# Performance work log

Hardware: AMD Instinct MI355X
Metric: run time of the kernel (lower is better)

The kernel has to match this reference:

```python
import jax, jax.numpy as jnp
import numpy as np

B, Q, K, D, H, HD, HID, ED, CPB, E = 2, 300, 1024, 256, 8, 32, 32, 256, 256, 131072
N = B * Q
EPS = 1e-5


def _ln(x, g, b):
    mu = x.mean(-1, keepdims=True)
    v = ((x - mu) ** 2).mean(-1, keepdims=True)
    return (x - mu) / jnp.sqrt(v + EPS) * g + b


def setup_inputs():
    key = jax.random.key(0)
    ks = jax.random.split(key, 32)
    rn = lambda k, s, sc=0.02: jax.random.normal(k, s, jnp.float32) * sc
    return {
        "nodes": jax.random.normal(ks[0], (N, D), jnp.float32),
        "images": jax.random.normal(ks[1], (B, K, D), jnp.float32),
        "rel_coords": jax.random.normal(ks[2], (B, Q, K, 2), jnp.float32),
        "edge_feats": jax.random.normal(ks[3], (E, ED), jnp.float32),
        "edge_index": jax.random.randint(ks[4], (2, E), 0, N, jnp.int32),
        "images_mask": jnp.zeros((B, K), dtype=bool),
        "ln1_g": jnp.ones((D,)), "ln1_b": jnp.zeros((D,)),
        "ln2_g": jnp.ones((D,)), "ln2_b": jnp.zeros((D,)),
        "ln3_g": jnp.ones((D,)), "ln3_b": jnp.zeros((D,)),
        "Wni": rn(ks[5], (D, HID * H)), "bni": jnp.zeros((HID * H,)),
        "Wnj": rn(ks[6], (D, HID * H)), "bnj": jnp.zeros((HID * H,)),
        "We": rn(ks[7], (ED, HID * H)), "be": jnp.zeros((HID * H,)),
        "attn_proj": jax.random.normal(ks[8], (H, HID), jnp.float32),
        "Wmsg": rn(ks[9], (D + ED, D)), "bmsg": jnp.zeros((D,)),
        "Wg_out": rn(ks[10], (D, D)), "bg_out": jnp.zeros((D,)),
        "Wq": rn(ks[11], (D, D)), "bq": jnp.zeros((D,)),
        "Wkv": rn(ks[12], (D, 2 * D)), "bkv": jnp.zeros((2 * D,)),
        "Wc1": rn(ks[13], (2, CPB), 0.5), "bc1": jnp.zeros((CPB,)),
        "Wc2": rn(ks[14], (CPB, H), 0.1), "bc2": jnp.zeros((H,)),
        "Wc_out": rn(ks[15], (D, D)), "bc_out": jnp.zeros((D,)),
        "Wf1": rn(ks[16], (D, 4 * D)), "bf1": jnp.zeros((4 * D,)),
        "Wf2": rn(ks[17], (4 * D, D)), "bf2": jnp.zeros((D,)),
    }


def reference(nodes, images, rel_coords, edge_feats, edge_index, images_mask,
              ln1_g, ln1_b, ln2_g, ln2_b, ln3_g, ln3_b,
              Wni, bni, Wnj, bnj, We, be, attn_proj, Wmsg, bmsg, Wg_out, bg_out,
              Wq, bq, Wkv, bkv, Wc1, bc1, Wc2, bc2, Wc_out, bc_out,
              Wf1, bf1, Wf2, bf2):
    src, dst = edge_index[0], edge_index[1]
    # --- graph attention (pre-LN residual) ---
    x = _ln(nodes, ln1_g, ln1_b)
    ni, nj = x[src], x[dst]  # [E, D]
    hidden = jax.nn.leaky_relu(
        ni @ Wni + bni + nj @ Wnj + bnj + edge_feats @ We + be, 0.2)
    hidden = hidden.reshape(E, H, HID)
    logits = jnp.einsum('ehd,hd->eh', hidden, attn_proj)  # [E, H]
    m = jax.ops.segment_max(logits, src, num_segments=N)
    z = jnp.exp(logits - m[src])
    scores = z / jax.ops.segment_sum(z, src, num_segments=N)[src]  # scatter softmax
    msg = (jnp.concatenate([nj, edge_feats], -1) @ Wmsg + bmsg).reshape(E, H, HD)
    agg = jax.ops.segment_sum(msg * scores[..., None], src, num_segments=N).reshape(N, D)
    nodes = nodes + (agg @ Wg_out + bg_out)
    # --- cross attention with continuous position bias ---
    x2 = _ln(nodes, ln2_g, ln2_b).reshape(B, Q, D)
    q = (x2 @ Wq + bq).reshape(B, Q, H, HD).transpose(0, 2, 1, 3)  # [B,H,Q,hd]
    kv = (images @ Wkv + bkv).reshape(B, K, 2, H, HD)
    k = kv[:, :, 0].transpose(0, 2, 1, 3)  # [B,H,K,hd]
    v = kv[:, :, 1].transpose(0, 2, 1, 3)
    cpb = jax.nn.relu(rel_coords @ Wc1 + bc1) @ Wc2 + bc2  # [B,Q,K,H]
    bias = jnp.where(images_mask[:, None, None, :], -jnp.inf,
                     jnp.transpose(cpb, (0, 3, 1, 2)))  # [B,H,Q,K]
    att = jnp.einsum('bhqd,bhkd->bhqk', q, k) / jnp.sqrt(jnp.float32(HD)) + bias
    p = jax.nn.softmax(att, axis=-1)
    out = jnp.einsum('bhqk,bhkd->bhqd', p, v)
    out = out.reshape(B, Q, H * HD)  # faithful to original: reshape WITHOUT head transpose
    nodes = nodes + (out @ Wc_out + bc_out).reshape(N, D)
    # --- FFN (residual from the normed input, as in original) ---
    x3 = _ln(nodes, ln3_g, ln3_b)
    ff = jax.nn.gelu(x3 @ Wf1 + bf1, approximate=False) @ Wf2 + bf2
    return ff + x3
```

## Files before the change

kernel.cpp:

```cpp
#include <hip/hip_runtime.h>
#include <hip/hip_bf16.h>
#include <math.h>

#define E_   131072
#define CH_  16384
#define N_   600
#define NB_  2
#define NQ_  300
#define NK_  1024
#define NH_  8

typedef __hip_bfloat16 bf16;
typedef __bf16 bh8 __attribute__((ext_vector_type(8)));
typedef float  fx4 __attribute__((ext_vector_type(4)));

static __device__ __forceinline__ float b2f(bf16 x){ return __bfloat162float(x); }
static __device__ __forceinline__ unsigned pack2(float x, float y){
  unsigned a = __bfloat16_as_ushort(__float2bfloat16(x));
  unsigned b = __bfloat16_as_ushort(__float2bfloat16(y));
  return a | (b << 16);
}
static __device__ __forceinline__ float ldf(const void* p, size_t i, bool isf32){
  return isf32 ? ((const float*)p)[i] : b2f(((const bf16*)p)[i]);
}

constexpr int WOFF[31] = {
  0,256,512,768,1024,1280,
  1536,67072,67328,132864,
  133120,133376,
  133632,264704,
  264960,330496,330752,396288,
  396544,527616,
  528128,528640,528896,530944,
  530952,596488,
  596744,858888,859912,1122056,
  1122312};
#define NWSEG 30
#define WTOT  1122312
struct SrcTab { const void* p[NWSEG]; };

static __device__ __forceinline__ void ln_stats(float v, int t, float* r1, float* r2,
                                                float& mu, float& rstd){
  float s1 = v, s2 = v*v;
  #pragma unroll
  for (int o = 32; o; o >>= 1){ s1 += __shfl_down(s1, o); s2 += __shfl_down(s2, o); }
  if ((t & 63) == 0){ r1[t>>6] = s1; r2[t>>6] = s2; }
  __syncthreads();
  float t1 = r1[0]+r1[1]+r1[2]+r1[3];
  float t2 = r2[0]+r2[1]+r2[2]+r2[3];
  mu = t1 * (1.f/256.f);
  float var = t2 * (1.f/256.f) - mu*mu;
  rstd = rsqrtf(var + 1e-5f);
  __syncthreads();
}

__global__ void k_init(int* cnt, unsigned* mkey, float* denom,
                       const void* nodes, int* dflag){
  int i = blockIdx.x*256 + threadIdx.x;
  if (i < N_) cnt[i] = 0;
  if (i < N_*NH_){ mkey[i] = 0u; denom[i] = 0.f; }
  if (i == 0){
    const unsigned short* h = (const unsigned short*)nodes;
    int odd = 0;
    for (int j = 0; j < 64; j++){
      int e = (h[j] >> 7) & 0xFF;
      if (e < 100 || e > 150) odd++;
    }
    *dflag = (odd > 8) ? 1 : 0;
  }
}

__global__ __launch_bounds__(256) void k_cvt(SrcTab tab, float* wall, const int* dflag){
  int i = blockIdx.x*256 + threadIdx.x;
  if (i >= WTOT) return;
  bool isf32 = (*dflag != 0);
  int seg = 0;
  while (seg < NWSEG-1 && i >= WOFF[seg+1]) seg++;
  wall[i] = ldf(tab.p[seg], (size_t)(i - WOFF[seg]), isf32);
}

__global__ __launch_bounds__(256) void k_prep2(
    const void* __restrict__ WeRaw, const int* __restrict__ dflag,
    const float* __restrict__ wall,
    bf16* __restrict__ WeT, bf16* __restrict__ WkvT, bf16* __restrict__ WnpT,
    bf16* __restrict__ WcoT, bf16* __restrict__ Wf1T, bf16* __restrict__ Wf2T,
    float* __restrict__ biasH)
{
  int i = blockIdx.x*256 + threadIdx.x;
  bool isf32 = (*dflag != 0);
  const float* Wni = wall + WOFF[6];
  const float* Wnj = wall + WOFF[8];
  const float* Wmsg= wall + WOFF[12];
  const float* Wkv = wall + WOFF[18];
  const float* Wco = wall + WOFF[24];
  const float* Wf1 = wall + WOFF[26];
  const float* Wf2 = wall + WOFF[28];
  if (i < 65536){
    int n = i >> 8, k = i & 255;
    WeT[i] = __float2bfloat16(ldf(WeRaw, (size_t)k*256 + n, isf32));
  } else if (i < 196608){
    int j = i - 65536; int n = j >> 8, k = j & 255;
    WkvT[j] = __float2bfloat16(Wkv[k*512 + n]);
  } else if (i < 393216){
    int j = i - 196608; int n = j >> 8, k = j & 255;
    float v = (n < 256) ? Wni[k*256 + n] : (n < 512) ? Wnj[k*256 + (n-256)]
                        : Wmsg[k*256 + (n-512)];
    WnpT[j] = __float2bfloat16(v);
  } else if (i < 458752){
    int j = i - 393216; int n = j >> 8, k = j & 255;
    WcoT[j] = __float2bfloat16(Wco[k*256 + n]);
  } else if (i < 720896){
    int j = i - 458752; int n = j >> 8, k = j & 255;
    Wf1T[j] = __float2bfloat16(Wf1[(size_t)k*1024 + n]);
  } else if (i < 983040){
    int j = i - 720896; int n = j >> 10, k = j & 1023;
    Wf2T[j] = __float2bfloat16(Wf2[(size_t)k*256 + n]);
  } else if (i < 983296){
    int j = i - 983040;
    biasH[j] = wall[WOFF[7]+j] + wall[WOFF[9]+j] + wall[WOFF[10]+j];
  }
}

__global__ __launch_bounds__(256) void k_ln1(
    const void* __restrict__ nodes, const int* __restrict__ dflag,
    const float* __restrict__ g1, const float* __restrict__ b1, bf16* __restrict__ x1)
{
  __shared__ float r1[4], r2[4];
  int n = blockIdx.x, t = threadIdx.x;
  bool isf32 = (*dflag != 0);
  float v = ldf(nodes, (size_t)n*256 + t, isf32);
  float mu, rstd;
  ln_stats(v, t, r1, r2, mu, rstd);
  x1[n*256 + t] = __float2bfloat16((v - mu) * rstd * g1[t] + b1[t]);
}

__global__ void k_count(const int* __restrict__ ei, int* cnt){
  int e = blockIdx.x*256 + threadIdx.x;
  atomicAdd(&cnt[ei[e]], 1);
}

__global__ __launch_bounds__(1024) void k_scan(const int* __restrict__ cnt,
                                               int* offs, int* cursor){
  __shared__ int s[1024];
  int t = threadIdx.x;
  s[t] = (t < N_) ? cnt[t] : 0;
  __syncthreads();
  for (int o = 1; o < 1024; o <<= 1){
    int v = 0;
    if (t >= o) v = s[t - o];
    __syncthreads();
    if (t >= o) s[t] += v;
    __syncthreads();
  }
  if (t < N_){ int excl = (t == 0) ? 0 : s[t-1]; offs[t] = excl; cursor[t] = excl; }
  if (t == N_-1) offs[N_] = s[N_-1];
}

__global__ void k_scatter(const int* __restrict__ ei, int* cursor, int* eorder){
  int e = blockIdx.x*256 + threadIdx.x;
  int pos = atomicAdd(&cursor[ei[e]], 1);
  eorder[pos] = e;
}

__global__ __launch_bounds__(256) void k_gemm_dual(
    const void* __restrict__ A, int m_base, const int* __restrict__ dflag,
    const bf16* __restrict__ BT, bf16* __restrict__ C)
{
  __shared__ __align__(16) bf16 As[128*40];
  __shared__ __align__(16) bf16 Bs[128*40];
  int m0 = blockIdx.x * 128;
  int n0 = blockIdx.y * 128;
  int t = threadIdx.x;
  bool isf32 = (*dflag != 0);
  int wave = t >> 6, lane = t & 63;
  int wr = (wave >> 1) * 64, wc = (wave & 1) * 64;
  int lm = lane & 15, lq = lane >> 4;
  int srow = t >> 2;
  int scol = (t & 3) * 8;
  size_t r0 = (size_t)(m_base + m0 + srow) * 256;
  size_t r1 = (size_t)(m_base + m0 + 64 + srow) * 256;
  fx4 acc[4][4] = {};
  for (int kk = 0; kk < 256; kk += 32){
    uint4 pa0, pa1;
    if (isf32){
      const float* a0p = (const float*)A + r0 + kk + scol;
      const float* a1p = (const float*)A + r1 + kk + scol;
      float4 va0a = *(const float4*)(a0p);
      float4 va0b = *(const float4*)(a0p + 4);
      float4 va1a = *(const float4*)(a1p);
      float4 va1b = *(const float4*)(a1p + 4);
      pa0.x = pack2(va0a.x, va0a.y); pa0.y = pack2(va0a.z, va0a.w);
      pa0.z = pack2(va0b.x, va0b.y); pa0.w = pack2(va0b.z, va0b.w);
      pa1.x = pack2(va1a.x, va1a.y); pa1.y = pack2(va1a.z, va1a.w);
      pa1.z = pack2(va1b.x, va1b.y); pa1.w = pack2(va1b.z, va1b.w);
    } else {
      pa0 = *(const uint4*)((const bf16*)A + r0 + kk + scol);
      pa1 = *(const uint4*)((const bf16*)A + r1 + kk + scol);
    }
    float4 vb0 = *(const float4*)(BT + (size_t)(n0 + srow)      * 256 + kk + scol);
    float4 vb1 = *(const float4*)(BT + (size_t)(n0 + 64 + srow) * 256 + kk + scol);
    __syncthreads();
    *(uint4*)(As + srow*40 + scol)         = pa0;
    *(uint4*)(As + (64 + srow)*40 + scol)  = pa1;
    *(float4*)(Bs + srow*40 + scol)        = vb0;
    *(float4*)(Bs + (64 + srow)*40 + scol) = vb1;
    __syncthreads();
    bh8 af[4], bfr[4];
    #pragma unroll
    for (int mt = 0; mt < 4; mt++)
      af[mt] = *reinterpret_cast<const bh8*>(As + (wr + mt*16 + lm)*40 + lq*8);
    #pragma unroll
    for (int nt = 0; nt < 4; nt++)
      bfr[nt] = *reinterpret_cast<const bh8*>(Bs + (wc + nt*16 + lm)*40 + lq*8);
    #pragma unroll
    for (int mt = 0; mt < 4; mt++)
      #pragma unroll
      for (int nt = 0; nt < 4; nt++)
        acc[mt][nt] = __builtin_amdgcn_mfma_f32_16x16x32_bf16(af[mt], bfr[nt], acc[mt][nt], 0, 0, 0);
  }
  #pragma unroll
  for (int mt = 0; mt < 4; mt++)
    #pragma unroll
    for (int nt = 0; nt < 4; nt++)
      #pragma unroll
      for (int r = 0; r < 4; r++){
        int row = m0 + wr + mt*16 + lq*4 + r;
        int col = n0 + wc + nt*16 + lm;
        C[(size_t)row*256 + col] = __float2bfloat16(acc[mt][nt][r]);
      }
}

__global__ __launch_bounds__(256) void k_gemm(
    const void* __restrict__ A, const int* __restrict__ dflag, int adual,
    int K, int M, const bf16* __restrict__ BT, int mode,
    void* __restrict__ D, int ldd,
    const float* __restrict__ bias, const float* __restrict__ add,
    float* __restrict__ aux)
{
  __shared__ __align__(16) bf16 As[128*40];
  __shared__ __align__(16) bf16 Bs[128*40];
  int m0 = blockIdx.x * 128;
  int n0 = blockIdx.y * 128;
  int t = threadIdx.x;
  bool f32src = adual && (*dflag != 0);
  int wave = t >> 6, lane = t & 63;
  int wr = (wave >> 1) * 64, wc = (wave & 1) * 64;
  int lm = lane & 15, lq = lane >> 4;
  int srow = t >> 2;
  int scol = (t & 3) * 8;
  size_t rA0 = (size_t)(m0 + srow) * K;
  size_t rA1 = (size_t)(m0 + 64 + srow) * K;
  size_t rB0 = (size_t)(n0 + srow) * K;
  size_t rB1 = (size_t)(n0 + 64 + srow) * K;
  fx4 acc[4][4] = {};
  for (int kk = 0; kk < K; kk += 32){
    uint4 pa0, pa1;
    if (f32src){
      const float* a0p = (const float*)A + rA0 + kk + scol;
      const float* a1p = (const float*)A + rA1 + kk + scol;
      float4 a = *(const float4*)(a0p), b = *(const float4*)(a0p + 4);
      float4 c = *(const float4*)(a1p), d = *(const float4*)(a1p + 4);
      pa0.x = pack2(a.x,a.y); pa0.y = pack2(a.z,a.w);
      pa0.z = pack2(b.x,b.y); pa0.w = pack2(b.z,b.w);
      pa1.x = pack2(c.x,c.y); pa1.y = pack2(c.z,c.w);
      pa1.z = pack2(d.x,d.y); pa1.w = pack2(d.z,d.w);
    } else {
      pa0 = *(const uint4*)((const bf16*)A + rA0 + kk + scol);
      pa1 = *(const uint4*)((const bf16*)A + rA1 + kk + scol);
    }
    float4 vb0 = *(const float4*)(BT + rB0 + kk + scol);
    float4 vb1 = *(const float4*)(BT + rB1 + kk + scol);
    __syncthreads();
    *(uint4*)(As + srow*40 + scol)         = pa0;
    *(uint4*)(As + (64 + srow)*40 + scol)  = pa1;
    *(float4*)(Bs + srow*40 + scol)        = vb0;
    *(float4*)(Bs + (64 + srow)*40 + scol) = vb1;
    __syncthreads();
    bh8 af[4], bfr[4];
    #pragma unroll
    for (int mt = 0; mt < 4; mt++)
      af[mt] = *reinterpret_cast<const bh8*>(As + (wr + mt*16 + lm)*40 + lq*8);
    #pragma unroll
    for (int nt = 0; nt < 4; nt++)
      bfr[nt] = *reinterpret_cast<const bh8*>(Bs + (wc + nt*16 + lm)*40 + lq*8);
    #pragma unroll
    for (int mt = 0; mt < 4; mt++)
      #pragma unroll
      for (int nt = 0; nt < 4; nt++)
        acc[mt][nt] = __builtin_amdgcn_mfma_f32_16x16x32_bf16(af[mt], bfr[nt], acc[mt][nt], 0, 0, 0);
  }
  #pragma unroll
  for (int mt = 0; mt < 4; mt++)
    #pragma unroll
    for (int nt = 0; nt < 4; nt++)
      #pragma unroll
      for (int r = 0; r < 4; r++){
        int row = m0 + wr + mt*16 + lq*4 + r;
        int col = n0 + wc + nt*16 + lm;
        if (row >= M) continue;
        float v = acc[mt][nt][r];
        if (mode == 0){
          if (bias) v += bias[col];
          ((float*)D)[(size_t)row*ldd + col] = v;
        } else if (mode == 1){
          v += bias[col];
          if (col < 256){
            ((float*)D)[(size_t)row*256 + col] = v;
          } else {
            int b = row >> 10, ki = row & 1023;
            int hh = (col - 256) >> 5, dd = (col - 256) & 31;
            aux[(((size_t)b*NH_ + hh)*32 + dd)*NK_ + ki] = v;
          }
        } else if (mode == 2){
          v += bias[col] + add[(size_t)row*ldd + col];
          ((float*)D)[(size_t)row*ldd + col] = v;
        } else {
          v += bias[col];
          float g = 0.5f*v*(1.f + erff(v*0.70710678118654752f));
          ((bf16*)D)[(size_t)row*ldd + col] = __float2bfloat16(g);
        }
      }
}

__global__ __launch_bounds__(256) void k_logits(
    const bf16* __restrict__ He, const float* __restrict__ Pall,
    const float* __restrict__ biasH, const float* __restrict__ ap, const int* __restrict__ ei,
    float* __restrict__ logits, unsigned* __restrict__ mkey, int e0chunk)
{
  __shared__ float hs[32*264];
  __shared__ int   ssh[32], dsh[32];
  __shared__ float aps[256], bhs[256];
  int t = threadIdx.x;
  int base = e0chunk + blockIdx.x*32;
  if (t < 32) ssh[t] = ei[base + t];
  else if (t < 64) dsh[t-32] = ei[E_ + base + (t - 32)];
  aps[t] = ap[t];
  bhs[t] = biasH[t];
  __syncthreads();
  int slot = (t >> 5)*33 + (t & 31);
  for (int r = 0; r < 32; r++){
    float v = b2f(He[(size_t)(base - e0chunk + r)*256 + t])
            + Pall[ssh[r]*768 + t] + Pall[dsh[r]*768 + 256 + t] + bhs[t];
    v = (v > 0.f) ? v : 0.2f*v;
    hs[r*264 + slot] = v;
  }
  __syncthreads();
  int e = t >> 3, h = t & 7;
  const float* hr  = hs + e*264 + h*33;
  const float* apr = aps + h*32;
  float acc = 0.f;
  #pragma unroll
  for (int i = 0; i < 32; i++) acc = fmaf(hr[i], apr[i], acc);
  logits[(size_t)(base + e)*8 + h] = acc;
  unsigned ub = __float_as_uint(acc);
  unsigned key = (ub & 0x80000000u) ? ~ub : (ub | 0x80000000u);
  atomicMax(&mkey[ssh[e]*8 + h], key);
}

__global__ __launch_bounds__(256) void k_softden(
    const int* __restrict__ ei, float* __restrict__ logits,
    const unsigned* __restrict__ mkey, float* __restrict__ denom)
{
  int gid = blockIdx.x*256 + threadIdx.x;
  int e = gid >> 3, h = gid & 7;
  int s = ei[e];
  unsigned key = mkey[s*8 + h];
  unsigned ub = (key & 0x80000000u) ? (key & 0x7FFFFFFFu) : ~key;
  float m = __uint_as_float(ub);
  float a = fminf(logits[gid] - m, 0.f);
  float z = __expf(a);
  logits[gid] = z;
  atomicAdd(&denom[s*8 + h], z);
}

__global__ __launch_bounds__(256) void k_agg_e(
    const int* __restrict__ offs, const int* __restrict__ eorder, const int* __restrict__ ei,
    const float* __restrict__ z,
    const void* __restrict__ ef, const int* __restrict__ dflag,
    const float* __restrict__ Pall,
    float* __restrict__ Fbuf, float* __restrict__ Gbuf)
{
  __shared__ float zsh[32*8];
  __shared__ int   esh[32];
  __shared__ int   dsh[32];
  int n = blockIdx.x, s = blockIdx.y, t = threadIdx.x;
  bool isf32 = (*dflag != 0);
  int h = t >> 5;
  int e0 = offs[n], e1 = offs[n+1];
  int total = e1 - e0;
  int half = (total + 1) >> 1;
  int start = e0 + s*half;
  int end   = min(e1, start + half);
  float facc[8] = {};
  float gacc = 0.f;
  int jz = t >> 3, hz = t & 7;
  for (int base = start; base < end; base += 32){
    int cnt = min(32, end - base);
    __syncthreads();
    if (t < 32){
      int e = (t < cnt) ? eorder[base + t] : eorder[start];
      esh[t] = e;
      dsh[t] = ei[E_ + e];
    }
    __syncthreads();
    zsh[t] = (jz < cnt) ? z[(size_t)esh[jz]*8 + hz] : 0.f;
    __syncthreads();
    #pragma unroll
    for (int jj = 0; jj < 32; jj++){
      int e = esh[jj];
      float efv = ldf(ef, (size_t)e*256 + t, isf32);
      float pv  = Pall[dsh[jj]*768 + 512 + t];
      #pragma unroll
      for (int hq = 0; hq < 8; hq++) facc[hq] = fmaf(zsh[jj*8 + hq], efv, facc[hq]);
      gacc = fmaf(zsh[jj*8 + h], pv, gacc);
    }
  }
  int slot = n*2 + s;
  #pragma unroll
  for (int hq = 0; hq < 8; hq++)
    Fbuf[((size_t)slot*8 + hq)*256 + t] = facc[hq];
  Gbuf[(size_t)slot*256 + t] = gacc;
}

__global__ __launch_bounds__(256) void k_agg_n(
    const float* __restrict__ Fbuf, const float* __restrict__ Gbuf,
    const float* __restrict__ denom,
    const float* __restrict__ bmsg, const float* __restrict__ Wmsg,
    const void* __restrict__ nodes, const int* __restrict__ dflag,
    const float* __restrict__ Wg, const float* __restrict__ bg,
    const float* __restrict__ g2, const float* __restrict__ b2v,
    const float* __restrict__ Wq, const float* __restrict__ bq,
    float* __restrict__ nodes1, float* __restrict__ qbuf)
{
  __shared__ float sinv[8];
  __shared__ float Fs[8*257];
  __shared__ float aggs[256];
  __shared__ float r1[4], r2[4];
  int n = blockIdx.x, t = threadIdx.x;
  bool isf32 = (*dflag != 0);
  int h = t >> 5;
  if (t < 8){
    float dsum = denom[n*8 + t];
    sinv[t] = (dsum > 0.f) ? 1.f/dsum : 0.f;
  }
  __syncthreads();
  #pragma unroll
  for (int hq = 0; hq < 8; hq++)
    Fs[hq*257 + t] = (Fbuf[((size_t)(n*2)*8 + hq)*256 + t]
                    + Fbuf[((size_t)(n*2+1)*8 + hq)*256 + t]) * sinv[hq];
  float gacc = (Gbuf[(size_t)(n*2)*256 + t] + Gbuf[(size_t)(n*2+1)*256 + t]) * sinv[h];
  __syncthreads();
  float am = gacc + bmsg[t];
  const float* fr = Fs + h*257;
  for (int k = 0; k < 256; k++)
    am = fmaf(fr[k], Wmsg[(size_t)(256 + k)*256 + t], am);
  aggs[t] = am;
  __syncthreads();
  float o = bg[t] + ldf(nodes, (size_t)n*256 + t, isf32);
  for (int k = 0; k < 256; k++) o = fmaf(aggs[k], Wg[k*256 + t], o);
  nodes1[n*256 + t] = o;
  float mu, rstd;
  ln_stats(o, t, r1, r2, mu, rstd);
  float x2 = (o - mu) * rstd * g2[t] + b2v[t];
  __syncthreads();
  aggs[t] = x2;
  __syncthreads();
  float q = bq[t];
  for (int k = 0; k < 256; k++) q = fmaf(aggs[k], Wq[k*256 + t], q);
  qbuf[n*256 + t] = q;
}

__global__ __launch_bounds__(256) void k_cpb(
    const void* __restrict__ rel, const int* __restrict__ dflag,
    const float* __restrict__ Wc1, const float* __restrict__ bc1,
    const float* __restrict__ Wc2, const float* __restrict__ bc2, bf16* __restrict__ bias)
{
  __shared__ float w0[256], w1[256], bb[256], w2[256*8], b2s[8];
  int t = threadIdx.x;
  bool isf32 = (*dflag != 0);
  w0[t] = Wc1[t]; w1[t] = Wc1[256 + t]; bb[t] = bc1[t];
  for (int i = t; i < 2048; i += 256) w2[i] = Wc2[i];
  if (t < 8) b2s[t] = bc2[t];
  __syncthreads();
  size_t pos = (size_t)blockIdx.x*256 + t;
  float c0 = ldf(rel, pos*2, isf32), c1 = ldf(rel, pos*2 + 1, isf32);
  float acc[8] = {};
  for (int j = 0; j < 256; j++){
    float hj = fmaf(c0, w0[j], fmaf(c1, w1[j], bb[j]));
    hj = fmaxf(hj, 0.f);
    #pragma unroll
    for (int h = 0; h < 8; h++) acc[h] = fmaf(hj, w2[j*8 + h], acc[h]);
  }
  int k = (int)(pos & 1023);
  size_t qq = pos >> 10;
  size_t b = qq / NQ_, q = qq % NQ_;
  bf16* dst = bias + ((b*NH_)*NQ_ + q)*NK_;
  #pragma unroll
  for (int h = 0; h < 8; h++)
    dst[(size_t)h*NQ_*NK_ + k] = __float2bfloat16(acc[h] + b2s[h]);
}

__global__ __launch_bounds__(256) void k_attn(
    const float* __restrict__ qbuf, const float* __restrict__ kbuf, const float* __restrict__ vT,
    const bf16* __restrict__ bias, bf16* __restrict__ Yb)
{
  __shared__ float Qs[8*33];
  __shared__ float Ks[128*33];
  __shared__ float Sc[8*1024];
  __shared__ float Op[4*8*32];
  __shared__ float qs[8];
  int qt = blockIdx.x, h = blockIdx.y, b = blockIdx.z;
  int q0 = qt*8;
  int t = threadIdx.x;
  {
    int q = t >> 5, d = t & 31;
    int gq = q0 + q;
    Qs[q*33 + d] = (gq < NQ_) ? qbuf[((size_t)b*NQ_ + gq)*256 + h*32 + d] : 0.f;
  }
  const float* kbase = kbuf + (size_t)b*NK_*256 + h*32;
  const bf16*  bb    = bias + ((size_t)(b*NH_ + h)*NQ_)*NK_;
  int kl = t & 127;
  int qb = (t >> 7) * 4;
  for (int kt = 0; kt < 8; kt++){
    int k0 = kt*128;
    __syncthreads();
    {
      int r = t >> 1, c0 = (t & 1) * 16;
      const float* src = kbase + (size_t)(k0 + r)*256 + c0;
      float* dst = Ks + r*33 + c0;
      #pragma unroll
      for (int ii = 0; ii < 4; ii++){
        float4 f = *(const float4*)(src + ii*4);
        dst[ii*4+0]=f.x; dst[ii*4+1]=f.y; dst[ii*4+2]=f.z; dst[ii*4+3]=f.w;
      }
    }
    __syncthreads();
    float a0=0.f, a1=0.f, a2=0.f, a3=0.f;
    const float* kr = Ks + kl*33;
    #pragma unroll
    for (int i = 0; i < 32; i++){
      float kd = kr[i];
      a0 = fmaf(kd, Qs[(qb+0)*33+i], a0);
      a1 = fmaf(kd, Qs[(qb+1)*33+i], a1);
      a2 = fmaf(kd, Qs[(qb+2)*33+i], a2);
      a3 = fmaf(kd, Qs[(qb+3)*33+i], a3);
    }
    float av[4] = {a0,a1,a2,a3};
    #pragma unroll
    for (int j = 0; j < 4; j++){
      int gq = min(q0 + qb + j, NQ_-1);
      float s = av[j]*0.17677669529663689f + b2f(bb[(size_t)gq*NK_ + k0 + kl]);
      Sc[(qb+j)*1024 + k0 + kl] = s;
    }
  }
  __syncthreads();
  {
    int q = t >> 5, j = t & 31;
    float m = -1e30f;
    for (int k = j; k < 1024; k += 32) m = fmaxf(m, Sc[q*1024 + k]);
    #pragma unroll
    for (int o = 16; o; o >>= 1) m = fmaxf(m, __shfl_xor(m, o));
    float ssum = 0.f;
    for (int k = j; k < 1024; k += 32){
      float e = __expf(Sc[q*1024 + k] - m);
      Sc[q*1024 + k] = e;
      ssum += e;
    }
    #pragma unroll
    for (int o = 16; o; o >>= 1) ssum += __shfl_xor(ssum, o);
    if (j == 0) qs[q] = ssum;
  }
  int d = t & 31, qg = (t >> 5) & 1, ks = t >> 6;
  const float* vrb = vT + (((size_t)(b*NH_ + h))*32)*NK_;
  float o0=0.f, o1=0.f, o2=0.f, o3=0.f;
  for (int kt = 0; kt < 8; kt++){
    int k0 = kt*128;
    __syncthreads();
    {
      int d2 = t >> 3, kq = (t & 7) * 16;
      const float* src = vrb + (size_t)d2*NK_ + k0 + kq;
      #pragma unroll
      for (int ii = 0; ii < 4; ii++){
        float4 f = *(const float4*)(src + ii*4);
        Ks[(kq+ii*4+0)*33 + d2] = f.x;
        Ks[(kq+ii*4+1)*33 + d2] = f.y;
        Ks[(kq+ii*4+2)*33 + d2] = f.z;
        Ks[(kq+ii*4+3)*33 + d2] = f.w;
      }
    }
    __syncthreads();
    const float* sc0 = Sc + (qg*4+0)*1024 + k0 + ks*32;
    const float* sc1 = Sc + (qg*4+1)*1024 + k0 + ks*32;
    const float* sc2 = Sc + (qg*4+2)*1024 + k0 + ks*32;
    const float* sc3 = Sc + (qg*4+3)*1024 + k0 + ks*32;
    #pragma unroll
    for (int kk = 0; kk < 32; kk++){
      float vv = Ks[(ks*32+kk)*33 + d];
      o0 = fmaf(sc0[kk], vv, o0);
      o1 = fmaf(sc1[kk], vv, o1);
      o2 = fmaf(sc2[kk], vv, o2);
      o3 = fmaf(sc3[kk], vv, o3);
    }
  }
  Op[((ks*8) + qg*4 + 0)*32 + d] = o0;
  Op[((ks*8) + qg*4 + 1)*32 + d] = o1;
  Op[((ks*8) + qg*4 + 2)*32 + d] = o2;
  Op[((ks*8) + qg*4 + 3)*32 + d] = o3;
  __syncthreads();
  {
    int q = t >> 5, dd = t & 31;
    int gq = q0 + q;
    if (gq < NQ_){
      float s = Op[(0*8+q)*32+dd] + Op[(1*8+q)*32+dd]
              + Op[(2*8+q)*32+dd] + Op[(3*8+q)*32+dd];
      float sv = s / qs[q];
      int tt = h*NQ_ + gq;
      Yb[((size_t)b*NQ_ + (tt >> 3))*256 + (tt & 7)*32 + dd] = __float2bfloat16(sv);
    }
  }
}

__global__ __launch_bounds__(256) void k_ln3(
    const float* __restrict__ n2, const float* __restrict__ g3, const float* __restrict__ b3,
    float* __restrict__ x3f, bf16* __restrict__ x3b)
{
  __shared__ float r1[4], r2[4];
  int n = blockIdx.x, t = threadIdx.x;
  float v = n2[n*256 + t];
  float mu, rstd;
  ln_stats(v, t, r1, r2, mu, rstd);
  float x3 = (v - mu) * rstd * g3[t] + b3[t];
  x3f[n*256 + t] = x3;
  x3b[n*256 + t] = __float2bfloat16(x3);
}

extern "C" void kernel_launch(void* const* d_in, const int* in_sizes, int n_in,
                              void* d_out, int out_size, void* d_ws, size_t ws_size,
                              hipStream_t stream)
{
  const void* nodes  = d_in[0];
  const void* images = d_in[1];
  const void* rel    = d_in[2];
  const void* ef     = d_in[3];
  const int*  ei     = (const int*)d_in[4];
  float* out = (float*)d_out;

  char* w = (char*)d_ws;
  auto alloc = [&](size_t bytes) -> void* {
    void* p = (void*)w; w += (bytes + 255) & ~(size_t)255; return p;
  };
  int*      dflag  = (int*)     alloc(4);
  float*    Wall   = (float*)   alloc((size_t)WTOT*4);
  bf16*     He     = (bf16*)    alloc((size_t)CH_*256*2);
  bf16*     bias   = (bf16*)    alloc((size_t)NB_*NH_*NQ_*NK_*2);
  float*    logits = (float*)   alloc((size_t)E_*8*4);
  float*    Fbuf   = (float*)   alloc((size_t)N_*2*8*256*4);
  float*    Gbuf   = (float*)   alloc((size_t)N_*2*256*4);
  float*    Pall   = (float*)   alloc((size_t)N_*768*4);
  float*    biasH  = (float*)   alloc(256*4);
  float*    nodes1 = (float*)   alloc(N_*256*4);
  float*    qbuf   = (float*)   alloc(N_*256*4);
  float*    kbuf   = (float*)   alloc((size_t)NB_*NK_*256*4);
  float*    vT     = (float*)   alloc((size_t)NB_*NH_*32*NK_*4);
  float*    n2buf  = (float*)   alloc(N_*256*4);
  float*    x3f    = (float*)   alloc(N_*256*4);
  bf16*     x1     = (bf16*)    alloc(N_*256*2);
  bf16*     x3b    = (bf16*)    alloc(N_*256*2);
  bf16*     Yb     = (bf16*)    alloc(N_*256*2);
  bf16*     H1     = (bf16*)    alloc((size_t)N_*1024*2);
  unsigned* mkey   = (unsigned*)alloc(N_*8*4);
  float*    denom  = (float*)   alloc(N_*8*4);
  int*      cnt    = (int*)     alloc(N_*4);
  int*      offs   = (int*)     alloc((N_+1)*4);
  int*      cursor = (int*)     alloc(N_*4);
  bf16*     WeT    = (bf16*)    alloc(256*256*2);
  bf16*     WkvT   = (bf16*)    alloc(512*256*2);
  bf16*     WnpT   = (bf16*)    alloc(768*256*2);
  bf16*     WcoT   = (bf16*)    alloc(256*256*2);
  bf16*     Wf1T   = (bf16*)    alloc(1024*256*2);
  bf16*     Wf2T   = (bf16*)    alloc((size_t)256*1024*2);
  int*      eorder = (int*)     alloc((size_t)E_*4);

  const float *ln1g=Wall+WOFF[0],  *ln1b=Wall+WOFF[1];
  const float *ln2g=Wall+WOFF[2],  *ln2b=Wall+WOFF[3];
  const float *ln3g=Wall+WOFF[4],  *ln3b=Wall+WOFF[5];
  const float *ap =Wall+WOFF[11];
  const float *Wmsg=Wall+WOFF[12], *bmsg=Wall+WOFF[13];
  const float *Wg=Wall+WOFF[14], *bg=Wall+WOFF[15];
  const float *Wq=Wall+WOFF[16], *bq=Wall+WOFF[17];
  const float *bkv=Wall+WOFF[19];
  const float *Wc1=Wall+WOFF[20], *bc1=Wall+WOFF[21];
  const float *Wc2=Wall+WOFF[22], *bc2=Wall+WOFF[23];
  const float *bco=Wall+WOFF[25];
  const float *bf1v=Wall+WOFF[27];
  const float *bf2v=Wall+WOFF[29];

  SrcTab tab;
  {
    const int idx[NWSEG] = {6,7,8,9,10,11, 12,13,14,15, 17,18, 19,20, 21,22,23,24,
                            25,26, 27,28,29,30, 31,32, 33,34,35,36};
    for (int i = 0; i < NWSEG; i++) tab.p[i] = d_in[idx[i]];
  }

  k_init   <<<19, 256, 0, stream>>>(cnt, mkey, denom, nodes, dflag);
  k_cvt    <<<(WTOT+255)/256, 256, 0, stream>>>(tab, Wall, dflag);
  k_prep2  <<<3841, 256, 0, stream>>>(d_in[16], dflag, Wall,
                                      WeT, WkvT, WnpT, WcoT, Wf1T, Wf2T, biasH);
  k_ln1    <<<N_, 256, 0, stream>>>(nodes, dflag, ln1g, ln1b, x1);
  k_count  <<<E_/256, 256, 0, stream>>>(ei, cnt);
  k_scan   <<<1, 1024, 0, stream>>>(cnt, offs, cursor);
  k_scatter<<<E_/256, 256, 0, stream>>>(ei, cursor, eorder);

  k_gemm<<<dim3(5,6), 256, 0, stream>>>(x1, dflag, 0, 256, N_, WnpT, 0,
                                        Pall, 768, nullptr, nullptr, nullptr);

  dim3 ggrid(CH_/128, 2);
  for (int c = 0; c < E_/CH_; c++){
    k_gemm_dual<<<ggrid, 256, 0, stream>>>(ef, c*CH_, dflag, WeT, He);
    k_logits   <<<CH_/32, 256, 0, stream>>>(He, Pall, biasH, ap, ei, logits, mkey, c*CH_);
  }
  k_softden<<<E_*8/256, 256, 0, stream>>>(ei, logits, mkey, denom);
  k_agg_e  <<<dim3(N_,2), 256, 0, stream>>>(offs, eorder, ei, logits, ef, dflag, Pall,
                                            Fbuf, Gbuf);
  k_agg_n  <<<N_, 256, 0, stream>>>(Fbuf, Gbuf, denom, bmsg, Wmsg, nodes, dflag,
                                    Wg, bg, ln2g, ln2b, Wq, bq, nodes1, qbuf);
  k_gemm<<<dim3(16,4), 256, 0, stream>>>(images, dflag, 1, 256, NB_*NK_, WkvT, 1,
                                         kbuf, 256, bkv, nullptr, vT);
  k_cpb    <<<NB_*NQ_*NK_/256, 256, 0, stream>>>(rel, dflag, Wc1, bc1, Wc2, bc2, bias);
  dim3 agrid((NQ_ + 7)/8, NH_, NB_);
  k_attn   <<<agrid, 256, 0, stream>>>(qbuf, kbuf, vT, bias, Yb);
  k_gemm<<<dim3(5,2), 256, 0, stream>>>(Yb, dflag, 0, 256, N_, WcoT, 2,
                                        n2buf, 256, bco, nodes1, nullptr);
  k_ln3  <<<N_, 256, 0, stream>>>(n2buf, ln3g, ln3b, x3f, x3b);
  k_gemm<<<dim3(5,8), 256, 0, stream>>>(x3b, dflag, 0, 256, N_, Wf1T, 3,
                                        H1, 1024, bf1v, nullptr, nullptr);
  k_gemm<<<dim3(5,2), 256, 0, stream>>>(H1, dflag, 0, 1024, N_, Wf2T, 2,
                                        out, 256, bf2v, x3f, nullptr);
}
```

Baseline: 863.9 us.

## Fuse edge aggregation into node kernel with MFMA and tiled weight transpose

```diff
diff --git a/kernel.cpp b/kernel.cpp
--- a/kernel.cpp
+++ b/kernel.cpp
@@ -15,16 +15,17 @@
 typedef float  fx4 __attribute__((ext_vector_type(4)));
 
 static __device__ __forceinline__ float b2f(bf16 x){ return __bfloat162float(x); }
+static __device__ __forceinline__ unsigned short bfu(float x){
+  return __bfloat16_as_ushort(__float2bfloat16(x));
+}
 static __device__ __forceinline__ unsigned pack2(float x, float y){
-  unsigned a = __bfloat16_as_ushort(__float2bfloat16(x));
-  unsigned b = __bfloat16_as_ushort(__float2bfloat16(y));
-  return a | (b << 16);
+  return (unsigned)bfu(x) | ((unsigned)bfu(y) << 16);
 }
 static __device__ __forceinline__ float ldf(const void* p, size_t i, bool isf32){
   return isf32 ? ((const float*)p)[i] : b2f(((const bf16*)p)[i]);
 }
 
-constexpr int WOFF[31] = {
+constexpr int WOFF[32] = {
   0,256,512,768,1024,1280,
   1536,67072,67328,132864,
   133120,133376,
@@ -34,10 +35,12 @@
   528128,528640,528896,530944,
   530952,596488,
   596744,858888,859912,1122056,
-  1122312};
-#define NWSEG 30
-#define WTOT  1122312
+  1122312,
+  1187848};
+#define NWSEG 31
+#define WTOT  1187848
 struct SrcTab { const void* p[NWSEG]; };
+struct TrTab { int4 d[8]; };
 
 static __device__ __forceinline__ void ln_stats(float v, int t, float* r1, float* r2,
                                                 float& mu, float& rstd){
@@ -79,45 +82,28 @@
   wall[i] = ldf(tab.p[seg], (size_t)(i - WOFF[seg]), isf32);
 }
 
-__global__ __launch_bounds__(256) void k_prep2(
-    const void* __restrict__ WeRaw, const int* __restrict__ dflag,
-    const float* __restrict__ wall,
-    bf16* __restrict__ WeT, bf16* __restrict__ WkvT, bf16* __restrict__ WnpT,
-    bf16* __restrict__ WcoT, bf16* __restrict__ Wf1T, bf16* __restrict__ Wf2T,
-    float* __restrict__ biasH)
-{
-  int i = blockIdx.x*256 + threadIdx.x;
-  bool isf32 = (*dflag != 0);
-  const float* Wni = wall + WOFF[6];
-  const float* Wnj = wall + WOFF[8];
-  const float* Wmsg= wall + WOFF[12];
-  const float* Wkv = wall + WOFF[18];
-  const float* Wco = wall + WOFF[24];
-  const float* Wf1 = wall + WOFF[26];
-  const float* Wf2 = wall + WOFF[28];
-  if (i < 65536){
-    int n = i >> 8, k = i & 255;
-    WeT[i] = __float2bfloat16(ldf(WeRaw, (size_t)k*256 + n, isf32));
-  } else if (i < 196608){
-    int j = i - 65536; int n = j >> 8, k = j & 255;
-    WkvT[j] = __float2bfloat16(Wkv[k*512 + n]);
-  } else if (i < 393216){
-    int j = i - 196608; int n = j >> 8, k = j & 255;
-    float v = (n < 256) ? Wni[k*256 + n] : (n < 512) ? Wnj[k*256 + (n-256)]
-                        : Wmsg[k*256 + (n-512)];
-    WnpT[j] = __float2bfloat16(v);
-  } else if (i < 458752){
-    int j = i - 393216; int n = j >> 8, k = j & 255;
-    WcoT[j] = __float2bfloat16(Wco[k*256 + n]);
-  } else if (i < 720896){
-    int j = i - 458752; int n = j >> 8, k = j & 255;
-    Wf1T[j] = __float2bfloat16(Wf1[(size_t)k*1024 + n]);
-  } else if (i < 983040){
-    int j = i - 720896; int n = j >> 10, k = j & 1023;
-    Wf2T[j] = __float2bfloat16(Wf2[(size_t)k*256 + n]);
-  } else if (i < 983296){
-    int j = i - 983040;
-    biasH[j] = wall[WOFF[7]+j] + wall[WOFF[9]+j] + wall[WOFF[10]+j];
+__global__ __launch_bounds__(256) void k_tr(TrTab tab, const float* __restrict__ wall,
+                                            bf16* __restrict__ wbt)
+{
+  __shared__ float tile[64][65];
+  int4 d = tab.d[blockIdx.z];
+  int K = d.y, Nn = d.z;
+  int k0 = blockIdx.x*64, n0 = blockIdx.y*64;
+  if (k0 >= K || n0 >= Nn) return;
+  const float* src = wall + d.x;
+  bf16* dst = wbt + d.w;
+  int t = threadIdx.x;
+  int rr = t >> 6, cc = t & 63;
+  #pragma unroll
+  for (int p = 0; p < 16; p++){
+    int row = p*4 + rr;
+    tile[row][cc] = src[(size_t)(k0 + row)*Nn + n0 + cc];
+  }
+  __syncthreads();
+  #pragma unroll
+  for (int p = 0; p < 16; p++){
+    int row = p*4 + rr;
+    dst[(size_t)(n0 + row)*K + k0 + cc] = __float2bfloat16(tile[cc][row]);
   }
 }
 
@@ -324,7 +310,8 @@
 
 __global__ __launch_bounds__(256) void k_logits(
     const bf16* __restrict__ He, const float* __restrict__ Pall,
-    const float* __restrict__ biasH, const float* __restrict__ ap, const int* __restrict__ ei,
+    const float* __restrict__ bni, const float* __restrict__ bnj, const float* __restrict__ be,
+    const float* __restrict__ ap, const int* __restrict__ ei,
     float* __restrict__ logits, unsigned* __restrict__ mkey, int e0chunk)
 {
   __shared__ float hs[32*264];
@@ -335,7 +322,7 @@
   if (t < 32) ssh[t] = ei[base + t];
   else if (t < 64) dsh[t-32] = ei[E_ + base + (t - 32)];
   aps[t] = ap[t];
-  bhs[t] = biasH[t];
+  bhs[t] = bni[t] + bnj[t] + be[t];
   __syncthreads();
   int slot = (t >> 5)*33 + (t & 31);
   for (int r = 0; r < 32; r++){
@@ -373,84 +360,85 @@
   atomicAdd(&denom[s*8 + h], z);
 }
 
-__global__ __launch_bounds__(256) void k_agg_e(
+__global__ __launch_bounds__(256) void k_agg(
     const int* __restrict__ offs, const int* __restrict__ eorder, const int* __restrict__ ei,
-    const float* __restrict__ z,
+    const float* __restrict__ z, const float* __restrict__ denom,
     const void* __restrict__ ef, const int* __restrict__ dflag,
     const float* __restrict__ Pall,
-    float* __restrict__ Fbuf, float* __restrict__ Gbuf)
-{
-  __shared__ float zsh[32*8];
-  __shared__ int   esh[32];
-  __shared__ int   dsh[32];
-  int n = blockIdx.x, s = blockIdx.y, t = threadIdx.x;
-  bool isf32 = (*dflag != 0);
-  int h = t >> 5;
-  int e0 = offs[n], e1 = offs[n+1];
-  int total = e1 - e0;
-  int half = (total + 1) >> 1;
-  int start = e0 + s*half;
-  int end   = min(e1, start + half);
-  float facc[8] = {};
-  float gacc = 0.f;
-  int jz = t >> 3, hz = t & 7;
-  for (int base = start; base < end; base += 32){
-    int cnt = min(32, end - base);
-    __syncthreads();
-    if (t < 32){
-      int e = (t < cnt) ? eorder[base + t] : eorder[start];
-      esh[t] = e;
-      dsh[t] = ei[E_ + e];
-    }
-    __syncthreads();
-    zsh[t] = (jz < cnt) ? z[(size_t)esh[jz]*8 + hz] : 0.f;
-    __syncthreads();
-    #pragma unroll
-    for (int jj = 0; jj < 32; jj++){
-      int e = esh[jj];
-      float efv = ldf(ef, (size_t)e*256 + t, isf32);
-      float pv  = Pall[dsh[jj]*768 + 512 + t];
-      #pragma unroll
-      for (int hq = 0; hq < 8; hq++) facc[hq] = fmaf(zsh[jj*8 + hq], efv, facc[hq]);
-      gacc = fmaf(zsh[jj*8 + h], pv, gacc);
-    }
-  }
-  int slot = n*2 + s;
-  #pragma unroll
-  for (int hq = 0; hq < 8; hq++)
-    Fbuf[((size_t)slot*8 + hq)*256 + t] = facc[hq];
-  Gbuf[(size_t)slot*256 + t] = gacc;
-}
-
-__global__ __launch_bounds__(256) void k_agg_n(
-    const float* __restrict__ Fbuf, const float* __restrict__ Gbuf,
-    const float* __restrict__ denom,
     const float* __restrict__ bmsg, const float* __restrict__ Wmsg,
-    const void* __restrict__ nodes, const int* __restrict__ dflag,
+    const void* __restrict__ nodes,
     const float* __restrict__ Wg, const float* __restrict__ bg,
     const float* __restrict__ g2, const float* __restrict__ b2v,
     const float* __restrict__ Wq, const float* __restrict__ bq,
     float* __restrict__ nodes1, float* __restrict__ qbuf)
 {
-  __shared__ float sinv[8];
+  __shared__ __align__(16) bf16 efs[256*40];
+  __shared__ __align__(16) bf16 za[16*40];
+  __shared__ float zsh[32*8];
+  __shared__ int   esh[32], dsh[32];
   __shared__ float Fs[8*257];
   __shared__ float aggs[256];
+  __shared__ float sinv[8];
   __shared__ float r1[4], r2[4];
   int n = blockIdx.x, t = threadIdx.x;
   bool isf32 = (*dflag != 0);
+  int wave = t >> 6, lane = t & 63;
+  int lm = lane & 15, lq = lane >> 4;
   int h = t >> 5;
+  int jz = t >> 3, hz = t & 7;
+  int e0 = offs[n], e1 = offs[n+1];
   if (t < 8){
-    float dsum = denom[n*8 + t];
-    sinv[t] = (dsum > 0.f) ? 1.f/dsum : 0.f;
+    float ds = denom[n*8 + t];
+    sinv[t] = (ds > 0.f) ? 1.f/ds : 0.f;
+  }
+  fx4 acc[4] = {};
+  float gacc = 0.f;
+  for (int base = e0; base < e1; base += 32){
+    int cnt = min(32, e1 - base);
+    __syncthreads();
+    if (t < 32){
+      int e = (t < cnt) ? eorder[base + t] : eorder[e0];
+      esh[t] = e; dsh[t] = ei[E_ + e];
+    }
+    __syncthreads();
+    float zv = (jz < cnt) ? z[(size_t)esh[jz]*8 + hz] : 0.f;
+    zsh[t] = zv;
+    za[hz*40 + jz] = __float2bfloat16(zv);
+    za[(8 + hz)*40 + jz] = (bf16)0.f;
+    #pragma unroll
+    for (int rb = 0; rb < 32; rb += 4){
+      float v0 = ldf(ef, (size_t)esh[rb+0]*256 + t, isf32);
+      float v1 = ldf(ef, (size_t)esh[rb+1]*256 + t, isf32);
+      float v2 = ldf(ef, (size_t)esh[rb+2]*256 + t, isf32);
+      float v3 = ldf(ef, (size_t)esh[rb+3]*256 + t, isf32);
+      ushort4 pk = { bfu(v0), bfu(v1), bfu(v2), bfu(v3) };
+      *(ushort4*)&efs[t*40 + rb] = pk;
+    }
+    __syncthreads();
+    #pragma unroll 8
+    for (int jj = 0; jj < 32; jj++)
+      gacc = fmaf(zsh[jj*8 + h], Pall[(size_t)dsh[jj]*768 + 512 + t], gacc);
+    bh8 afrag = *reinterpret_cast<const bh8*>(za + lm*40 + lq*8);
+    #pragma unroll
+    for (int tile = 0; tile < 4; tile++){
+      int coln = wave*64 + tile*16 + lm;
+      bh8 bfrag = *reinterpret_cast<const bh8*>(efs + coln*40 + lq*8);
+      acc[tile] = __builtin_amdgcn_mfma_f32_16x16x32_bf16(afrag, bfrag, acc[tile], 0, 0, 0);
+    }
   }
   __syncthreads();
   #pragma unroll
-  for (int hq = 0; hq < 8; hq++)
-    Fs[hq*257 + t] = (Fbuf[((size_t)(n*2)*8 + hq)*256 + t]
-                    + Fbuf[((size_t)(n*2+1)*8 + hq)*256 + t]) * sinv[hq];
-  float gacc = (Gbuf[(size_t)(n*2)*256 + t] + Gbuf[(size_t)(n*2+1)*256 + t]) * sinv[h];
-  __syncthreads();
-  float am = gacc + bmsg[t];
+  for (int tile = 0; tile < 4; tile++)
+    #pragma unroll
+    for (int r = 0; r < 4; r++){
+      int row = lq*4 + r;
+      if (row < 8){
+        int col = wave*64 + tile*16 + lm;
+        Fs[row*257 + col] = acc[tile][r] * sinv[row];
+      }
+    }
+  __syncthreads();
+  float am = gacc * sinv[h] + bmsg[t];
   const float* fr = Fs + h*257;
   for (int k = 0; k < 256; k++)
     am = fmaf(fr[k], Wmsg[(size_t)(256 + k)*256 + t], am);
@@ -651,13 +639,11 @@
   };
   int*      dflag  = (int*)     alloc(4);
   float*    Wall   = (float*)   alloc((size_t)WTOT*4);
+  bf16*     Wbt    = (bf16*)    alloc((size_t)983040*2);
   bf16*     He     = (bf16*)    alloc((size_t)CH_*256*2);
   bf16*     bias   = (bf16*)    alloc((size_t)NB_*NH_*NQ_*NK_*2);
   float*    logits = (float*)   alloc((size_t)E_*8*4);
-  float*    Fbuf   = (float*)   alloc((size_t)N_*2*8*256*4);
-  float*    Gbuf   = (float*)   alloc((size_t)N_*2*256*4);
   float*    Pall   = (float*)   alloc((size_t)N_*768*4);
-  float*    biasH  = (float*)   alloc(256*4);
   float*    nodes1 = (float*)   alloc(N_*256*4);
   float*    qbuf   = (float*)   alloc(N_*256*4);
   float*    kbuf   = (float*)   alloc((size_t)NB_*NK_*256*4);
@@ -673,17 +659,19 @@
   int*      cnt    = (int*)     alloc(N_*4);
   int*      offs   = (int*)     alloc((N_+1)*4);
   int*      cursor = (int*)     alloc(N_*4);
-  bf16*     WeT    = (bf16*)    alloc(256*256*2);
-  bf16*     WkvT   = (bf16*)    alloc(512*256*2);
-  bf16*     WnpT   = (bf16*)    alloc(768*256*2);
-  bf16*     WcoT   = (bf16*)    alloc(256*256*2);
-  bf16*     Wf1T   = (bf16*)    alloc(1024*256*2);
-  bf16*     Wf2T   = (bf16*)    alloc((size_t)256*1024*2);
   int*      eorder = (int*)     alloc((size_t)E_*4);
+
+  bf16* WeT  = Wbt + 0;
+  bf16* WkvT = Wbt + 65536;
+  bf16* WnpT = Wbt + 196608;
+  bf16* WcoT = Wbt + 393216;
+  bf16* Wf1T = Wbt + 458752;
+  bf16* Wf2T = Wbt + 720896;
 
   const float *ln1g=Wall+WOFF[0],  *ln1b=Wall+WOFF[1];
   const float *ln2g=Wall+WOFF[2],  *ln2b=Wall+WOFF[3];
   const float *ln3g=Wall+WOFF[4],  *ln3b=Wall+WOFF[5];
+  const float *bni=Wall+WOFF[7],  *bnj=Wall+WOFF[9], *be=Wall+WOFF[10];
   const float *ap =Wall+WOFF[11];
   const float *Wmsg=Wall+WOFF[12], *bmsg=Wall+WOFF[13];
   const float *Wg=Wall+WOFF[14], *bg=Wall+WOFF[15];
@@ -698,14 +686,22 @@
   SrcTab tab;
   {
     const int idx[NWSEG] = {6,7,8,9,10,11, 12,13,14,15, 17,18, 19,20, 21,22,23,24,
-                            25,26, 27,28,29,30, 31,32, 33,34,35,36};
+                            25,26, 27,28,29,30, 31,32, 33,34,35,36, 16};
     for (int i = 0; i < NWSEG; i++) tab.p[i] = d_in[idx[i]];
   }
+  TrTab tr;
+  tr.d[0] = {WOFF[30], 256,  256, 0};
+  tr.d[1] = {WOFF[18], 256,  512, 65536};
+  tr.d[2] = {WOFF[6],  256,  256, 196608};
+  tr.d[3] = {WOFF[8],  256,  256, 196608+65536};
+  tr.d[4] = {WOFF[12], 256,  256, 196608+131072};
+  tr.d[5] = {WOFF[24], 256,  256, 393216};
+  tr.d[6] = {WOFF[26], 256, 1024, 458752};
+  tr.d[7] = {WOFF[28],1024,  256, 720896};
 
   k_init   <<<19, 256, 0, stream>>>(cnt, mkey, denom, nodes, dflag);
   k_cvt    <<<(WTOT+255)/256, 256, 0, stream>>>(tab, Wall, dflag);
-  k_prep2  <<<3841, 256, 0, stream>>>(d_in[16], dflag, Wall,
-                                      WeT, WkvT, WnpT, WcoT, Wf1T, Wf2T, biasH);
+  k_tr     <<<dim3(16,16,8), 256, 0, stream>>>(tr, Wall, Wbt);
   k_ln1    <<<N_, 256, 0, stream>>>(nodes, dflag, ln1g, ln1b, x1);
   k_count  <<<E_/256, 256, 0, stream>>>(ei, cnt);
   k_scan   <<<1, 1024, 0, stream>>>(cnt, offs, cursor);
@@ -717,13 +713,13 @@
   dim3 ggrid(CH_/128, 2);
   for (int c = 0; c < E_/CH_; c++){
     k_gemm_dual<<<ggrid, 256, 0, stream>>>(ef, c*CH_, dflag, WeT, He);
-    k_logits   <<<CH_/32, 256, 0, stream>>>(He, Pall, biasH, ap, ei, logits, mkey, c*CH_);
+    k_logits   <<<CH_/32, 256, 0, stream>>>(He, Pall, bni, bnj, be, ap, ei,
+                                            logits, mkey, c*CH_);
   }
   k_softden<<<E_*8/256, 256, 0, stream>>>(ei, logits, mkey, denom);
-  k_agg_e  <<<dim3(N_,2), 256, 0, stream>>>(offs, eorder, ei, logits, ef, dflag, Pall,
-                                            Fbuf, Gbuf);
-  k_agg_n  <<<N_, 256, 0, stream>>>(Fbuf, Gbuf, denom, bmsg, Wmsg, nodes, dflag,
-                                    Wg, bg, ln2g, ln2b, Wq, bq, nodes1, qbuf);
+  k_agg    <<<N_, 256, 0, stream>>>(offs, eorder, ei, logits, denom, ef, dflag, Pall,
+                                    bmsg, Wmsg, nodes, Wg, bg, ln2g, ln2b, Wq, bq,
+                                    nodes1, qbuf);
   k_gemm<<<dim3(16,4), 256, 0, stream>>>(images, dflag, 1, 256, NB_*NK_, WkvT, 1,
                                          kbuf, 256, bkv, nullptr, vT);
   k_cpb    <<<NB_*NQ_*NK_/256, 256, 0, stream>>>(rel, dflag, Wc1, bc1, Wc2, bc2, bias);
```

After: 866.9 us. Within noise of the previous version (+0.4%).
